# Kernel optimization log

Measured on AMD Instinct MI355X. Metric: run time of the kernel, lower is better.

Reference implementation:

```python
import jax, jax.numpy as jnp
import numpy as np

STRIDE = 1  # module init arg


def setup_inputs() -> dict:
    key = jax.random.key(0)
    k1, k2 = jax.random.split(key)
    x = jax.random.normal(k1, (16, 32, 256, 256), dtype=jnp.float32)
    kernel = jax.random.normal(k2, (32, 5, 5), dtype=jnp.float32) * 0.1
    return {"input": x, "kernel": kernel}


def _maxmin_conv(x, kernel, stride=STRIDE):
    # Max-min semifield convolution:
    #   out[b,oc,i,j] = max_{c,dy,dx} min(x_pad[b,c,i*s+dy,j*s+dx], k[oc,dy,dx])
    # Since min(., k) is monotone in x, the max over in-channels commutes:
    #   max_{c} min(x_c, k) == min(max_c x_c, k)
    # so we reduce channels once up front (same math, far less memory).
    K = kernel.shape[-1]
    p = K - 1
    top = p // 2
    bot = p - top  # calculate_padding(): left=top=floor(p/2), right=bottom=p-top
    xmax = jnp.max(x, axis=1)  # [B, H, W]
    xp = jnp.pad(xmax, ((0, 0), (top, bot), (top, bot)), constant_values=-np.inf)
    B, Hp, Wp = xp.shape
    Ho = (Hp - K) // stride + 1
    Wo = (Wp - K) // stride + 1
    OC = kernel.shape[0]
    acc = jnp.full((B, OC, Ho, Wo), -np.inf, dtype=x.dtype)
    for dy in range(K):  # fixed small K*K loop over kernel taps
        for dx in range(K):
            patch = xp[:, dy:dy + stride * Ho:stride, dx:dx + stride * Wo:stride]  # [B,Ho,Wo]
            cand = jnp.minimum(patch[:, None, :, :], kernel[None, :, dy, dx, None, None])
            acc = jnp.maximum(acc, cand)
    return acc


def reference(input, kernel):
    return _maxmin_conv(input, kernel)
```

## Files before the change

### kernel.cpp

```cpp
#include <hip/hip_runtime.h>
#include <math.h>


#define BATCH 16
#define CH    32
#define OCH   32
#define HH    256
#define WW    256
#define HWSZ  (HH * WW)
#define TW    32
#define TH    16
#define LH    20
#define LW    42
#define NWGB  (BATCH * (HH / TH) * (WW / TW))

typedef float floatx4 __attribute__((ext_vector_type(4)));

__global__ void sort_taps_kernel(const float* __restrict__ kk, float2* __restrict__ ent) {
    int t = threadIdx.x;
    if (t >= OCH * 25) return;
    int oc = t / 25, i = t % 25;
    float ki = kk[oc * 25 + i];
    int rank = 0;
#pragma unroll
    for (int j = 0; j < 25; ++j) {
        float kj = kk[oc * 25 + j];
        rank += (kj > ki) || (kj == ki && j < i);
    }
    int dy = i / 5, dx = i % 5;
    int off = 4 * (dy * LW + dx);
    ent[oc * 26 + rank] = make_float2(ki, __int_as_float(off));
    if (i == 0) ent[oc * 26 + 25] = make_float2(-INFINITY, __int_as_float(0));
}

__global__ __launch_bounds__(256) void chanmax_kernel(const float* __restrict__ x,
                                                      float* __restrict__ xm) {
    int i4 = blockIdx.x * blockDim.x + threadIdx.x;
    int b  = i4 >> 14;
    int r  = i4 & 16383;
    const float4* base = (const float4*)x + (size_t)b * (CH * (HWSZ / 4)) + r;

    float4 v[16];
#pragma unroll
    for (int j = 0; j < 16; ++j) v[j] = base[(size_t)j * (HWSZ / 4)];
    float4 m = v[0];
#pragma unroll
    for (int j = 1; j < 16; ++j) {
        m.x = fmaxf(m.x, v[j].x); m.y = fmaxf(m.y, v[j].y);
        m.z = fmaxf(m.z, v[j].z); m.w = fmaxf(m.w, v[j].w);
    }
#pragma unroll
    for (int j = 0; j < 16; ++j) v[j] = base[(size_t)(16 + j) * (HWSZ / 4)];
#pragma unroll
    for (int j = 0; j < 16; ++j) {
        m.x = fmaxf(m.x, v[j].x); m.y = fmaxf(m.y, v[j].y);
        m.z = fmaxf(m.z, v[j].z); m.w = fmaxf(m.w, v[j].w);
    }
    ((float4*)xm)[i4] = m;
}

__global__ __launch_bounds__(256, 2) void conv_kernel(const float* __restrict__ xm,
                                                      const float2* __restrict__ gent,
                                                      float* __restrict__ out) {
    __shared__ float xmt[LH][LW];
    __shared__ float2 ent[OCH * 26];
    int tid = threadIdx.x;
    int bid = blockIdx.x;
    int swz = (bid & 7) * (NWGB >> 3) + (bid >> 3);
    int b   = swz >> 7;
    int t2  = swz & 127;
    int ty  = t2 >> 3;
    int tx  = t2 & 7;

    const float NI = -INFINITY;

    for (int i = tid; i < OCH * 26; i += 256) ent[i] = gent[i];

    if (tid < 200) {
        int pr = tid / 10;
        int pc = tid % 10;
        int c4 = tx * 8 - 1 + pc;
        int rw = ty * TH - 2 + pr;
        bool valid = (c4 >= 0) && (c4 < WW / 4) && (rw >= 0) && (rw < HH);
        int c4c = c4 < 0 ? 0 : (c4 > WW / 4 - 1 ? WW / 4 - 1 : c4);
        int rwc = rw < 0 ? 0 : (rw > HH - 1 ? HH - 1 : rw);
        float4 m = *((const float4*)xm + (size_t)b * (HWSZ / 4)
                     + (size_t)rwc * (WW / 4) + c4c);
        if (!valid) { m.x = NI; m.y = NI; m.z = NI; m.w = NI; }
        *(float2*)&xmt[pr][4 * pc]     = make_float2(m.x, m.y);
        *(float2*)&xmt[pr][4 * pc + 2] = make_float2(m.z, m.w);
    }
    __syncthreads();

    int xg = tid & 7;
    int rg = (tid >> 3) & 7;
    int wv = __builtin_amdgcn_readfirstlane(tid >> 6);

    const char* r0p = (const char*)&xmt[2 * rg][4 * xg + 2];
    const char* r1p = (const char*)&xmt[2 * rg + 1][4 * xg + 2];

    size_t obase = (size_t)(b * OCH + wv * 8) * HWSZ
                 + (size_t)(ty * TH + 2 * rg) * WW + tx * TW + 4 * xg;

    for (int o = 0; o < 8; ++o) {
        const float2* E = &ent[(wv * 8 + o) * 26];
        float a00 = NI, a01 = NI, a02 = NI, a03 = NI;
        float a10 = NI, a11 = NI, a12 = NI, a13 = NI;

        for (int i = 0; i < 25; ++i) {
            float2 e  = E[i];
            float  kn = E[i + 1].x;
            float  kv = e.x;
            int    off = __float_as_int(e.y);
            const float* p0 = (const float*)(r0p + off);
            const float* p1 = (const float*)(r1p + off);
            a00 = fmaxf(a00, fminf(p0[0], kv));
            a01 = fmaxf(a01, fminf(p0[1], kv));
            a02 = fmaxf(a02, fminf(p0[2], kv));
            a03 = fmaxf(a03, fminf(p0[3], kv));
            a10 = fmaxf(a10, fminf(p1[0], kv));
            a11 = fmaxf(a11, fminf(p1[1], kv));
            a12 = fmaxf(a12, fminf(p1[2], kv));
            a13 = fmaxf(a13, fminf(p1[3], kv));
            float mn = fminf(fminf(fminf(a00, a01), fminf(a02, a03)),
                             fminf(fminf(a10, a11), fminf(a12, a13)));
            if (__all(mn >= kn)) break;
        }

        float* op = out + obase + (size_t)o * HWSZ;
        floatx4 o0 = { a00, a01, a02, a03 };
        floatx4 o1 = { a10, a11, a12, a13 };
        __builtin_nontemporal_store(o0, (floatx4*)op);
        __builtin_nontemporal_store(o1, (floatx4*)(op + WW));
    }
}

extern "C" void kernel_launch(void* const* d_in, const int* in_sizes, int n_in,
                              void* d_out, int out_size, void* d_ws, size_t ws_size,
                              hipStream_t stream) {
    const float* x  = (const float*)d_in[0];
    const float* kk = (const float*)d_in[1];
    float* out      = (float*)d_out;
    float2* ent     = (float2*)d_ws;
    float*  xm      = (float*)((char*)d_ws + 8192);

    sort_taps_kernel<<<1, OCH * 25, 0, stream>>>(kk, ent);
    chanmax_kernel<<<BATCH * HWSZ / 4 / 256, 256, 0, stream>>>(x, xm);
    conv_kernel<<<NWGB, 256, 0, stream>>>(xm, ent, out);
}
```

Baseline: 64.02 us.

## Give each wavefront its own 8x32 tile covering all output channels

Each wavefront now owns its own 8x32 spatial tile with a private LDS halo buffer and computes all 32 output channels for it, one pixel-quad per lane. Before, a workgroup shared a 16x32 tile and split the output channels across wavefronts. The tile load now waits only on the wavefront's own LDS writes instead of a workgroup barrier. This aims to cut cross-wave synchronisation and make the early-exit vote cover fewer pixels, so it exits sooner. The cost is more halo overhead per output and fewer accumulators per thread, which means less ILP per tap.

```diff
diff --git a/kernel.cpp b/kernel.cpp
--- a/kernel.cpp
+++ b/kernel.cpp
@@ -8,11 +8,9 @@
 #define HH    256
 #define WW    256
 #define HWSZ  (HH * WW)
-#define TW    32
-#define TH    16
-#define LH    20
-#define LW    42
-#define NWGB  (BATCH * (HH / TH) * (WW / TW))
+#define LH    12
+#define LW    44
+#define NWGB  1024
 
 typedef float floatx4 __attribute__((ext_vector_type(4)));
 
@@ -62,76 +60,66 @@
 __global__ __launch_bounds__(256, 2) void conv_kernel(const float* __restrict__ xm,
                                                       const float2* __restrict__ gent,
                                                       float* __restrict__ out) {
-    __shared__ float xmt[LH][LW];
+    __shared__ float xs[4][LH][LW];
     __shared__ float2 ent[OCH * 26];
-    int tid = threadIdx.x;
-    int bid = blockIdx.x;
-    int swz = (bid & 7) * (NWGB >> 3) + (bid >> 3);
-    int b   = swz >> 7;
-    int t2  = swz & 127;
-    int ty  = t2 >> 3;
-    int tx  = t2 & 7;
+    int tid  = threadIdx.x;
+    int wv   = tid >> 6;
+    int lane = tid & 63;
+    int bid  = blockIdx.x;
+    int swz  = (bid & 7) * (NWGB >> 3) + (bid >> 3);
+    int tile = swz * 4 + wv;
+    int b    = tile >> 8;
+    int t2   = tile & 255;
+    int ty   = t2 >> 3;
+    int tx   = t2 & 7;
 
     const float NI = -INFINITY;
 
     for (int i = tid; i < OCH * 26; i += 256) ent[i] = gent[i];
-
-    if (tid < 200) {
-        int pr = tid / 10;
-        int pc = tid % 10;
-        int c4 = tx * 8 - 1 + pc;
-        int rw = ty * TH - 2 + pr;
-        bool valid = (c4 >= 0) && (c4 < WW / 4) && (rw >= 0) && (rw < HH);
-        int c4c = c4 < 0 ? 0 : (c4 > WW / 4 - 1 ? WW / 4 - 1 : c4);
-        int rwc = rw < 0 ? 0 : (rw > HH - 1 ? HH - 1 : rw);
-        float4 m = *((const float4*)xm + (size_t)b * (HWSZ / 4)
-                     + (size_t)rwc * (WW / 4) + c4c);
-        if (!valid) { m.x = NI; m.y = NI; m.z = NI; m.w = NI; }
-        *(float2*)&xmt[pr][4 * pc]     = make_float2(m.x, m.y);
-        *(float2*)&xmt[pr][4 * pc + 2] = make_float2(m.z, m.w);
-    }
     __syncthreads();
 
-    int xg = tid & 7;
-    int rg = (tid >> 3) & 7;
-    int wv = __builtin_amdgcn_readfirstlane(tid >> 6);
+    float* Ls = &xs[wv][0][0];
+    const float4* xb4 = (const float4*)xm + (size_t)b * (HWSZ / 4);
+#pragma unroll
+    for (int gi = 0; gi < 2; ++gi) {
+        int g = lane + 64 * gi;
+        if (g < 120) {
+            int pr = g / 10, pc = g % 10;
+            int c4 = tx * 8 - 1 + pc;
+            int rw = ty * 8 - 2 + pr;
+            bool valid = (c4 >= 0) && (c4 < WW / 4) && (rw >= 0) && (rw < HH);
+            int c4c = c4 < 0 ? 0 : (c4 > WW / 4 - 1 ? WW / 4 - 1 : c4);
+            int rwc = rw < 0 ? 0 : (rw > HH - 1 ? HH - 1 : rw);
+            float4 m = xb4[(size_t)rwc * (WW / 4) + c4c];
+            if (!valid) { m.x = NI; m.y = NI; m.z = NI; m.w = NI; }
+            *(float4*)(Ls + pr * LW + 4 * pc) = m;
+        }
+    }
+    asm volatile("s_waitcnt lgkmcnt(0)" ::: "memory");
 
-    const char* r0p = (const char*)&xmt[2 * rg][4 * xg + 2];
-    const char* r1p = (const char*)&xmt[2 * rg + 1][4 * xg + 2];
+    int xg = lane & 7;
+    int rw = lane >> 3;
+    const char* wbase = (const char*)(Ls + rw * LW + 4 * xg + 2);
+    size_t obase = (size_t)b * OCH * HWSZ + (size_t)(ty * 8 + rw) * WW
+                 + tx * 32 + 4 * xg;
 
-    size_t obase = (size_t)(b * OCH + wv * 8) * HWSZ
-                 + (size_t)(ty * TH + 2 * rg) * WW + tx * TW + 4 * xg;
-
-    for (int o = 0; o < 8; ++o) {
-        const float2* E = &ent[(wv * 8 + o) * 26];
-        float a00 = NI, a01 = NI, a02 = NI, a03 = NI;
-        float a10 = NI, a11 = NI, a12 = NI, a13 = NI;
-
+    for (int o = 0; o < OCH; ++o) {
+        const float2* E = &ent[o * 26];
+        float a0 = NI, a1 = NI, a2 = NI, a3 = NI;
         for (int i = 0; i < 25; ++i) {
             float2 e  = E[i];
             float  kn = E[i + 1].x;
             float  kv = e.x;
-            int    off = __float_as_int(e.y);
-            const float* p0 = (const float*)(r0p + off);
-            const float* p1 = (const float*)(r1p + off);
-            a00 = fmaxf(a00, fminf(p0[0], kv));
-            a01 = fmaxf(a01, fminf(p0[1], kv));
-            a02 = fmaxf(a02, fminf(p0[2], kv));
-            a03 = fmaxf(a03, fminf(p0[3], kv));
-            a10 = fmaxf(a10, fminf(p1[0], kv));
-            a11 = fmaxf(a11, fminf(p1[1], kv));
-            a12 = fmaxf(a12, fminf(p1[2], kv));
-            a13 = fmaxf(a13, fminf(p1[3], kv));
-            float mn = fminf(fminf(fminf(a00, a01), fminf(a02, a03)),
-                             fminf(fminf(a10, a11), fminf(a12, a13)));
+            const float* p = (const float*)(wbase + __float_as_int(e.y));
+            a0 = fmaxf(a0, fminf(p[0], kv));
+            a1 = fmaxf(a1, fminf(p[1], kv));
+            a2 = fmaxf(a2, fminf(p[2], kv));
+            a3 = fmaxf(a3, fminf(p[3], kv));
+            float mn = fminf(fminf(a0, a1), fminf(a2, a3));
             if (__all(mn >= kn)) break;
         }
-
-        float* op = out + obase + (size_t)o * HWSZ;
-        floatx4 o0 = { a00, a01, a02, a03 };
-        floatx4 o1 = { a10, a11, a12, a13 };
-        __builtin_nontemporal_store(o0, (floatx4*)op);
-        __builtin_nontemporal_store(o1, (floatx4*)(op + WW));
+        floatx4 ov = { a0, a1, a2, a3 };
+        __builtin_nontemporal_store(ov, (floatx4*)(out + obase + (size_t)o * HWSZ));
     }
 }
 
```

New measurement: 62.86 us. About the same (-1.8%).
